# Performance work log

Measured on AMD Instinct MI355X. Metric: run time of the kernel, lower is better.

The kernel has to match this reference:

```python
import jax, jax.numpy as jnp
import numpy as np

N, T, C, H = 32, 512, 768, 1536  # batch, seq_len, dim, int(dim*expand)


def setup_inputs() -> dict:
    key = jax.random.key(0)
    ks = jax.random.split(key, 10)
    sc = lambda fan: 1.0 / np.sqrt(fan)
    return {
        "x_seq": jax.random.normal(ks[0], (N, T, C), jnp.float32),
        "sup_seq": jax.random.uniform(ks[1], (N, T, 1), jnp.float32),
        # torch nn.Linear weights are [out, in]; y = x @ W.T + b
        "W_in": jax.random.normal(ks[2], (C, C), jnp.float32) * sc(C),
        "W_out": jax.random.normal(ks[3], (C, C), jnp.float32) * sc(C),
        "W_bg": jax.random.normal(ks[4], (C, C), jnp.float32) * sc(C),
        "b_bg": jax.random.normal(ks[5], (C,), jnp.float32) * 0.01,
        "W_sg": jax.random.normal(ks[6], (C, 1), jnp.float32),
        "b_sg": jax.random.normal(ks[7], (C,), jnp.float32) * 0.01,
        "W_f1": jax.random.normal(ks[8], (H, C), jnp.float32) * sc(C),
        "b_f1": jnp.zeros((H,), jnp.float32),
        "W_f2": jax.random.normal(ks[9], (C, H), jnp.float32) * sc(H),
        "b_f2": jnp.zeros((C,), jnp.float32),
    }


def reference(x_seq, sup_seq, W_in, W_out, W_bg, b_bg, W_sg, b_sg, W_f1, b_f1, W_f2, b_f2):
    # in_proj (no bias)
    x = jnp.einsum('ntc,dc->ntd', x_seq, W_in)                      # [N,T,C]
    # per-step FFN with residual (exact erf GELU, matching torch default)
    h = jax.nn.gelu(jnp.einsum('ntc,hc->nth', x, W_f1) + b_f1, approximate=False)
    xt = x + jnp.einsum('nth,ch->ntc', h, W_f2) + b_f2              # [N,T,C]
    # input-dependent gate (base_gate * sup_to_gate)
    g = jax.nn.sigmoid(jnp.einsum('ntc,dc->ntd', xt, W_bg) + b_bg)
    g = g * jax.nn.sigmoid(jnp.einsum('nto,do->ntd', sup_seq, W_sg) + b_sg)
    # linear recurrence s_t = (1-g_t)*s_{t-1} + g_t*xt_t, s_0 = 0 -> associative scan
    a = 1.0 - g
    b = g * xt

    def combine(c1, c2):
        a1, b1 = c1
        a2, b2 = c2
        return a2 * a1, a2 * b1 + b2

    _, s = jax.lax.associative_scan(combine, (a, b), axis=1)        # [N,T,C]
    return jnp.einsum('ntc,dc->ntd', s, W_out)
```

## Files before the change

kernel.cpp:

```cpp
#include <hip/hip_runtime.h>
#include <hip/hip_bf16.h>
#include <math.h>

typedef __bf16 bf16;
typedef __attribute__((ext_vector_type(8))) __bf16 bf16x8;
typedef __attribute__((ext_vector_type(4))) __bf16 bf16x4;
typedef __attribute__((ext_vector_type(4))) float f32x4;

constexpr int BM = 128, BN = 128, BK = 32;

enum { EPI_PLAIN = 0, EPI_GELU = 1, EPI_RES = 2, EPI_GATE = 3 };

__device__ __forceinline__ void async16(const void* g, void* l) {
  __builtin_amdgcn_global_load_lds(
      (const __attribute__((address_space(1))) void*)g,
      (__attribute__((address_space(3))) void*)l, 16, 0, 0);
}

template <typename CT, int EPI>
__global__ __launch_bounds__(256, 2) void gemm_bt_a(
    const bf16* __restrict__ A, const bf16* __restrict__ B, CT* __restrict__ C,
    const float* __restrict__ bias, const bf16* __restrict__ resid,
    const float* __restrict__ sup, const float* __restrict__ wsg,
    const float* __restrict__ bsg, int M, int N, int K) {
  __shared__ bf16 As[BM * BK];
  __shared__ bf16 Bs[BN * BK];

  const int tid = threadIdx.x;
  const int bm = blockIdx.x, bn = blockIdx.y;
  const int lane = tid & 63;
  const int wv = tid >> 6;
  const int wm = (wv >> 1) * 64, wn = (wv & 1) * 64;
  const int quad = lane >> 4, l16 = lane & 15;

  f32x4 acc[4][4];
#pragma unroll
  for (int i = 0; i < 4; i++)
#pragma unroll
    for (int j = 0; j < 4; j++) acc[i][j] = f32x4{0.f, 0.f, 0.f, 0.f};

  const bf16* Ab = A + (size_t)(bm * BM) * K;
  const bf16* Bb = B + (size_t)(bn * BN) * K;
  const int srow = tid >> 2, sk8 = (tid & 3) * 8;

  for (int kk = 0; kk < K; kk += BK) {
#pragma unroll
    for (int it = 0; it < 2; ++it) {
      int row = it * 64 + srow;
      async16(Ab + (size_t)row * K + kk + sk8, &As[(it * 256 + wv * 64) * 8]);
    }
#pragma unroll
    for (int it = 0; it < 2; ++it) {
      int row = it * 64 + srow;
      async16(Bb + (size_t)row * K + kk + sk8, &Bs[(it * 256 + wv * 64) * 8]);
    }
    __syncthreads();

    bf16x8 af[4], bfr[4];
#pragma unroll
    for (int i = 0; i < 4; i++) af[i] = *(const bf16x8*)&As[(wm + i * 16 + l16) * BK + quad * 8];
#pragma unroll
    for (int j = 0; j < 4; j++) bfr[j] = *(const bf16x8*)&Bs[(wn + j * 16 + l16) * BK + quad * 8];
#pragma unroll
    for (int i = 0; i < 4; i++)
#pragma unroll
      for (int j = 0; j < 4; j++)
        acc[i][j] = __builtin_amdgcn_mfma_f32_16x16x32_bf16(af[i], bfr[j], acc[i][j], 0, 0, 0);
    __syncthreads();
  }

#pragma unroll
  for (int i = 0; i < 4; i++) {
    int row0 = bm * BM + wm + i * 16 + quad * 4;
#pragma unroll
    for (int j = 0; j < 4; j++) {
      int col = bn * BN + wn + j * 16 + l16;
#pragma unroll
      for (int r = 0; r < 4; r++) {
        int row = row0 + r;
        size_t idx = (size_t)row * N + col;
        float v = acc[i][j][r];
        if constexpr (EPI == EPI_PLAIN) {
          C[idx] = (CT)v;
        } else if constexpr (EPI == EPI_GELU) {
          v += bias[col];
          float gl = 0.5f * v * (1.0f + erff(v * 0.70710678118654752f));
          C[idx] = (CT)gl;
        } else if constexpr (EPI == EPI_RES) {
          v += bias[col] + (float)resid[idx];
          C[idx] = (CT)v;
        } else {
          v += bias[col];
          float g1 = 1.0f / (1.0f + expf(-v));
          float z = sup[row] * wsg[col] + bsg[col];
          float g2 = 1.0f / (1.0f + expf(-z));
          C[idx] = (CT)(g1 * g2);
        }
      }
    }
  }
}

constexpr int SC_CH = 32, SC_NCH = 16, SC_CW = 32;

__global__ __launch_bounds__(512) void scan2_kernel(const float* __restrict__ g,
                                                    const bf16* __restrict__ xt,
                                                    bf16* __restrict__ s, int T, int C) {
  __shared__ float lA[SC_NCH][SC_CW];
  __shared__ float lB[SC_NCH][SC_CW];
  __shared__ float lC[SC_NCH][SC_CW];
  const int cl = threadIdx.x & (SC_CW - 1);
  const int ch = threadIdx.x / SC_CW;
  const int c = blockIdx.x * SC_CW + cl;
  const int n = blockIdx.y;
  const size_t base = ((size_t)n * T + ch * SC_CH) * C + c;

  float a_arr[SC_CH], sl[SC_CH];
  float A = 1.f, B = 0.f;
#pragma unroll
  for (int t = 0; t < SC_CH; ++t) {
    size_t idx = base + (size_t)t * C;
    float gv = g[idx], xv = (float)xt[idx];
    float at = 1.0f - gv;
    a_arr[t] = at;
    B = at * B + gv * xv;
    sl[t] = B;
    A *= at;
  }
  lA[ch][cl] = A;
  lB[ch][cl] = B;
  __syncthreads();
  if (ch == 0) {
    float carry = 0.f;
#pragma unroll
    for (int j = 0; j < SC_NCH; ++j) {
      lC[j][cl] = carry;
      carry = lA[j][cl] * carry + lB[j][cl];
    }
  }
  __syncthreads();
  const float carry = lC[ch][cl];
  float P = 1.f;
#pragma unroll
  for (int t = 0; t < SC_CH; ++t) {
    P *= a_arr[t];
    s[base + (size_t)t * C] = (bf16)(sl[t] + P * carry);
  }
}

__global__ __launch_bounds__(256) void cvt5_kernel(
    const float* s0, bf16* d0, int n0, const float* s1, bf16* d1, int n1,
    const float* s2, bf16* d2, int n2, const float* s3, bf16* d3, int n3,
    const float* s4, bf16* d4, int n4) {
  const float* s; bf16* d; int n;
  switch (blockIdx.y) {
    case 0: s = s0; d = d0; n = n0; break;
    case 1: s = s1; d = d1; n = n1; break;
    case 2: s = s2; d = d2; n = n2; break;
    case 3: s = s3; d = d3; n = n3; break;
    default: s = s4; d = d4; n = n4; break;
  }
  int i = blockIdx.x * 256 + threadIdx.x;
  if (i < n) d[i] = (bf16)s[i];
}

__global__ __launch_bounds__(256) void cvtx_kernel(const float* __restrict__ in,
                                                   bf16* __restrict__ out, int n4) {
  int i = blockIdx.x * 256 + threadIdx.x;
  if (i < n4) {
    f32x4 v = *(const f32x4*)(in + (size_t)i * 4);
    bf16x4 b;
    b[0] = (bf16)v[0]; b[1] = (bf16)v[1]; b[2] = (bf16)v[2]; b[3] = (bf16)v[3];
    *(bf16x4*)(out + (size_t)i * 4) = b;
  }
}

extern "C" void kernel_launch(void* const* d_in, const int* in_sizes, int n_in,
                              void* d_out, int out_size, void* d_ws, size_t ws_size,
                              hipStream_t stream) {
  const float* x_seq = (const float*)d_in[0];
  const float* sup = (const float*)d_in[1];
  const float* W_in = (const float*)d_in[2];
  const float* W_out = (const float*)d_in[3];
  const float* W_bg = (const float*)d_in[4];
  const float* b_bg = (const float*)d_in[5];
  const float* W_sg = (const float*)d_in[6];
  const float* b_sg = (const float*)d_in[7];
  const float* W_f1 = (const float*)d_in[8];
  const float* b_f1 = (const float*)d_in[9];
  const float* W_f2 = (const float*)d_in[10];
  const float* b_f2 = (const float*)d_in[11];

  const int Nb = 32, T = 512, C = 768, H = 1536;
  const int M = Nb * T;

  char* ws = (char*)d_ws;
  size_t off = 0;
  auto alloc = [&](size_t bytes) {
    void* p = ws + off;
    off += (bytes + 255) & ~(size_t)255;
    return p;
  };
  bf16* Win_bf = (bf16*)alloc((size_t)C * C * 2);
  bf16* Wf1_bf = (bf16*)alloc((size_t)H * C * 2);
  bf16* Wf2_bf = (bf16*)alloc((size_t)C * H * 2);
  bf16* Wbg_bf = (bf16*)alloc((size_t)C * C * 2);
  bf16* Wout_bf = (bf16*)alloc((size_t)C * C * 2);
  bf16* xs_bf = (bf16*)alloc((size_t)M * C * 2);
  bf16* x_bf = (bf16*)alloc((size_t)M * C * 2);
  bf16* h_bf = (bf16*)alloc((size_t)M * H * 2);
  bf16* xt_bf = (bf16*)alloc((size_t)M * C * 2);
  float* g_f = (float*)alloc((size_t)M * C * 4);
  bf16* s_bf = x_bf;

  cvt5_kernel<<<dim3((H * C + 255) / 256, 5), 256, 0, stream>>>(
      W_in, Win_bf, C * C, W_f1, Wf1_bf, H * C, W_f2, Wf2_bf, C * H,
      W_bg, Wbg_bf, C * C, W_out, Wout_bf, C * C);
  cvtx_kernel<<<(M * C / 4 + 255) / 256, 256, 0, stream>>>(x_seq, xs_bf, M * C / 4);

  dim3 blk(256);
  gemm_bt_a<bf16, EPI_PLAIN><<<dim3(M / BM, C / BN), blk, 0, stream>>>(
      xs_bf, Win_bf, x_bf, nullptr, nullptr, nullptr, nullptr, nullptr, M, C, C);
  gemm_bt_a<bf16, EPI_GELU><<<dim3(M / BM, H / BN), blk, 0, stream>>>(
      x_bf, Wf1_bf, h_bf, b_f1, nullptr, nullptr, nullptr, nullptr, M, H, C);
  gemm_bt_a<bf16, EPI_RES><<<dim3(M / BM, C / BN), blk, 0, stream>>>(
      h_bf, Wf2_bf, xt_bf, b_f2, x_bf, nullptr, nullptr, nullptr, M, C, H);
  gemm_bt_a<float, EPI_GATE><<<dim3(M / BM, C / BN), blk, 0, stream>>>(
      xt_bf, Wbg_bf, g_f, b_bg, nullptr, sup, W_sg, b_sg, M, C, C);
  scan2_kernel<<<dim3(C / SC_CW, Nb), dim3(SC_CW * SC_NCH), 0, stream>>>(
      g_f, xt_bf, s_bf, T, C);
  gemm_bt_a<float, EPI_PLAIN><<<dim3(M / BM, C / BN), blk, 0, stream>>>(
      s_bf, Wout_bf, (float*)d_out, nullptr, nullptr, nullptr, nullptr, nullptr, M, C, C);
}
```

Measured before the change: 366.0 us.

## Double GEMM K-tile to 64 with fragment-ordered LDS layout

Raises the GEMM K tile from 32 to 64 so each iteration runs two MFMA k-steps per pair of barriers, halving the loop trip count and the synchronization overhead. The async global-to-LDS staging is remapped so LDS is stored in a 16-row by 8-element fragment-major order that each MFMA fragment reads contiguously, which should avoid bank conflicts on the ds_read. LDS use per block doubles, which may affect occupancy. The epilogue GELU/residual code is also lightly refactored into a helper.

```diff
diff --git a/kernel.cpp b/kernel.cpp
--- a/kernel.cpp
+++ b/kernel.cpp
@@ -7,7 +7,7 @@
 typedef __attribute__((ext_vector_type(4))) __bf16 bf16x4;
 typedef __attribute__((ext_vector_type(4))) float f32x4;
 
-constexpr int BM = 128, BN = 128, BK = 32;
+constexpr int BM = 128, BN = 128, BK = 64;
 
 enum { EPI_PLAIN = 0, EPI_GELU = 1, EPI_RES = 2, EPI_GATE = 3 };
 
@@ -15,6 +15,10 @@
   __builtin_amdgcn_global_load_lds(
       (const __attribute__((address_space(1))) void*)g,
       (__attribute__((address_space(3))) void*)l, 16, 0, 0);
+}
+
+__device__ __forceinline__ float epi_apply_gelu(float v) {
+  return 0.5f * v * (1.0f + erff(v * 0.70710678118654752f));
 }
 
 template <typename CT, int EPI>
@@ -41,31 +45,38 @@
 
   const bf16* Ab = A + (size_t)(bm * BM) * K;
   const bf16* Bb = B + (size_t)(bn * BN) * K;
-  const int srow = tid >> 2, sk8 = (tid & 3) * 8;
+  const int s_l16 = tid & 15;
+  const int s_hi = tid >> 7;
+  const int s_g8 = ((tid >> 4) & 7) * 8;
 
   for (int kk = 0; kk < K; kk += BK) {
 #pragma unroll
-    for (int it = 0; it < 2; ++it) {
-      int row = it * 64 + srow;
-      async16(Ab + (size_t)row * K + kk + sk8, &As[(it * 256 + wv * 64) * 8]);
-    }
-#pragma unroll
-    for (int it = 0; it < 2; ++it) {
-      int row = it * 64 + srow;
-      async16(Bb + (size_t)row * K + kk + sk8, &Bs[(it * 256 + wv * 64) * 8]);
+    for (int it = 0; it < 4; ++it) {
+      int row = (it * 2 + s_hi) * 16 + s_l16;
+      async16(Ab + (size_t)row * K + kk + s_g8, &As[(it * 256 + wv * 64) * 8]);
+    }
+#pragma unroll
+    for (int it = 0; it < 4; ++it) {
+      int row = (it * 2 + s_hi) * 16 + s_l16;
+      async16(Bb + (size_t)row * K + kk + s_g8, &Bs[(it * 256 + wv * 64) * 8]);
     }
     __syncthreads();
 
-    bf16x8 af[4], bfr[4];
-#pragma unroll
-    for (int i = 0; i < 4; i++) af[i] = *(const bf16x8*)&As[(wm + i * 16 + l16) * BK + quad * 8];
-#pragma unroll
-    for (int j = 0; j < 4; j++) bfr[j] = *(const bf16x8*)&Bs[(wn + j * 16 + l16) * BK + quad * 8];
-#pragma unroll
-    for (int i = 0; i < 4; i++)
+#pragma unroll
+    for (int ks = 0; ks < 2; ++ks) {
+      bf16x8 af[4], bfr[4];
+#pragma unroll
+      for (int i = 0; i < 4; i++)
+        af[i] = *(const bf16x8*)&As[(((wm >> 4) + i) * 128 + (ks * 4 + quad) * 16 + l16) * 8];
 #pragma unroll
       for (int j = 0; j < 4; j++)
-        acc[i][j] = __builtin_amdgcn_mfma_f32_16x16x32_bf16(af[i], bfr[j], acc[i][j], 0, 0, 0);
+        bfr[j] = *(const bf16x8*)&Bs[(((wn >> 4) + j) * 128 + (ks * 4 + quad) * 16 + l16) * 8];
+#pragma unroll
+      for (int i = 0; i < 4; i++)
+#pragma unroll
+        for (int j = 0; j < 4; j++)
+          acc[i][j] = __builtin_amdgcn_mfma_f32_16x16x32_bf16(af[i], bfr[j], acc[i][j], 0, 0, 0);
+    }
     __syncthreads();
   }
 
@@ -83,12 +94,9 @@
         if constexpr (EPI == EPI_PLAIN) {
           C[idx] = (CT)v;
         } else if constexpr (EPI == EPI_GELU) {
-          v += bias[col];
-          float gl = 0.5f * v * (1.0f + erff(v * 0.70710678118654752f));
-          C[idx] = (CT)gl;
+          C[idx] = (CT)epi_apply_gelu(v + bias[col]);
         } else if constexpr (EPI == EPI_RES) {
-          v += bias[col] + (float)resid[idx];
-          C[idx] = (CT)v;
+          C[idx] = (CT)(v + bias[col] + (float)resid[idx]);
         } else {
           v += bias[col];
           float g1 = 1.0f / (1.0f + expf(-v));
```

Measured after the change: 465.6 us. 27.2% more time.
